# Performance work log

Hardware: AMD Instinct MI355X
Metric: run time of the kernel (lower is better)

The kernel has to match this reference:

```python
import jax, jax.numpy as jnp
import numpy as np
from jax import lax

B, T, A = 64, 1024, 512
FILTERS, K = 32, 31
PAD = (K - 1) // 2


def setup_inputs() -> dict:
    key = jax.random.key(0)
    ks = jax.random.split(key, 12)
    return {
        "encoder_seq_proj": jax.random.normal(ks[0], (B, T, A), jnp.float32),
        "query": jax.random.normal(ks[1], (B, A), jnp.float32),
        "cumulative": jax.random.uniform(ks[2], (B, T), jnp.float32),
        "attention": jax.random.uniform(ks[3], (B, T), jnp.float32),
        "alpha": jax.random.uniform(ks[4], (B, T), jnp.float32),
        "conv_w": jax.random.normal(ks[5], (FILTERS, 2, K), jnp.float32) * 0.1,
        "L_w": jax.random.normal(ks[6], (A, FILTERS), jnp.float32) * 0.1,
        "L_b": jax.random.normal(ks[7], (A,), jnp.float32) * 0.1,
        "W_w": jax.random.normal(ks[8], (A, A), jnp.float32) * 0.05,
        "W_b": jax.random.normal(ks[9], (A,), jnp.float32) * 0.05,
        "v_w": jax.random.normal(ks[10], (1, A), jnp.float32) * 0.05,
        "t": 1,
        "phone_len": jax.random.randint(ks[11], (B,), 1, T + 1).astype(jnp.int64),
    }


def reference(encoder_seq_proj, query, cumulative, attention, alpha,
              conv_w, L_w, L_b, W_w, W_b, v_w, t, phone_len):
    # attention mask from phone lengths (set at init, reused each step)
    mask = (jnp.arange(T)[None, :] < phone_len[:, None]).astype(encoder_seq_proj.dtype)
    # processed query: [B, 1, A]
    pq = (query @ W_w.T + W_b)[:, None, :]
    # location features: stack cumulative + previous attention -> [B, 2, T]
    loc = jnp.stack([cumulative, attention], axis=1)
    conv_out = lax.conv_general_dilated(
        loc, conv_w, window_strides=(1,), padding=[(PAD, PAD)],
        dimension_numbers=("NCH", "OIH", "NCH"))  # [B, F, T]
    ploc = jnp.einsum("bft,af->bta", conv_out, L_w) + L_b  # [B, T, A]
    # additive energies -> [B, T]
    u = jnp.einsum("bta,a->bt", jnp.tanh(pq + encoder_seq_proj + ploc), v_w[0])
    s = jax.nn.sigmoid(u)
    scores = s / jnp.sum(s, axis=1, keepdims=True)
    att = scores * mask
    # forward-attention recursion (enable_forward_bias=True path)
    shift_alpha = jnp.pad(alpha[:, :-1], ((0, 0), (1, 0)))
    dual_alpha = jnp.pad(alpha[:, :-2], ((0, 0), (2, 0)))
    new_alpha = (shift_alpha + dual_alpha + alpha + 1e-7) * att
    new_alpha = new_alpha / jnp.sum(new_alpha, axis=-1, keepdims=True)
    return new_alpha[:, None, :]  # [B, 1, T]
```

## Files before the change

kernel.cpp:

```cpp
#include <hip/hip_runtime.h>

#define NB 64
#define NT 1024
#define NA 512
#define NF 32
#define KW 31
#define PADW 15
#define TB 32

typedef __fp16 half2v __attribute__((ext_vector_type(2)));

__device__ __forceinline__ float fast_tanh(float x) {
    float e = __builtin_amdgcn_exp2f(x * 2.885390081777927f);
    return 1.0f - 2.0f * __builtin_amdgcn_rcpf(1.0f + e);
}
__device__ __forceinline__ float fast_sigmoid(float u) {
    return __builtin_amdgcn_rcpf(1.0f + __builtin_amdgcn_exp2f(-u * 1.4426950408889634f));
}
__device__ __forceinline__ unsigned pkrtz(float a, float b) {
    half2v h = __builtin_amdgcn_cvt_pkrtz(a, b);
    return __builtin_bit_cast(unsigned, h);
}
__device__ __forceinline__ float fdot2u(unsigned cv, unsigned lw, float acc) {
#if __has_builtin(__builtin_amdgcn_fdot2)
    return __builtin_amdgcn_fdot2(__builtin_bit_cast(half2v, cv),
                                  __builtin_bit_cast(half2v, lw), acc, false);
#else
    half2v a = __builtin_bit_cast(half2v, cv), b = __builtin_bit_cast(half2v, lw);
    return acc + (float)a.x * (float)b.x + (float)a.y * (float)b.y;
#endif
}

__global__ __launch_bounds__(256) void lsa_pq(
    const float* __restrict__ query, const float* __restrict__ Ww,
    const float* __restrict__ Wb, const float* __restrict__ convw,
    float* __restrict__ pq, float* __restrict__ cwT)
{
    if (blockIdx.x == 0) {
        for (int i = threadIdx.x; i < NF * 2 * KW; i += 256) {
            int f = i / (2 * KW);
            int r = i - f * 2 * KW;
            int c = r / KW;
            int k = r - c * KW;
            cwT[(c * KW + k) * NF + f] = convw[i];
        }
    }
    __shared__ float qs[NA];
    int tid = threadIdx.x;
    int b = blockIdx.x >> 1;
    int a0 = (blockIdx.x & 1) * 256;
    qs[tid]       = query[b * NA + tid];
    qs[tid + 256] = query[b * NA + tid + 256];
    __syncthreads();
    int a = a0 + tid;
    const float4* wr = (const float4*)(Ww + (long)a * NA);
    float acc  = Wb[a];
    float acc2 = 0.f;
#pragma unroll 8
    for (int k = 0; k < NA / 4; ++k) {
        float4 w = wr[k];
        float4 q4 = *(const float4*)(qs + 4 * k);
        acc  += w.x * q4.x + w.y * q4.y;
        acc2 += w.z * q4.z + w.w * q4.w;
    }
    pq[b * NA + a] = acc + acc2;
}

__global__ __launch_bounds__(256, 4) void lsa_main(
    const float* __restrict__ enc, const float* __restrict__ cum,
    const float* __restrict__ att, const float* __restrict__ cwT,
    const float* __restrict__ Lw, const float* __restrict__ Lb,
    const float* __restrict__ vw, const float* __restrict__ pq,
    float* __restrict__ sout)
{
    __shared__ float cum_s[TB + 30];
    __shared__ float att_s[TB + 30];
    __shared__ unsigned cvsh[TB][20];
    __shared__ float wred[4][33];

    int tid = threadIdx.x;
    int b  = blockIdx.x >> 5;
    int t0 = (blockIdx.x & 31) * TB;

    int a0 = 2 * tid;
    const float4* lp = (const float4*)(Lw + (long)a0 * NF);
    float4 lf[16];
#pragma unroll
    for (int i = 0; i < 16; ++i) lf[i] = lp[i];
    float c0 = pq[b * NA + a0]     + Lb[a0];
    float c1 = pq[b * NA + a0 + 1] + Lb[a0 + 1];
    float vx = vw[a0], vy = vw[a0 + 1];

    if (tid < TB + 30) {
        int t = t0 - PADW + tid;
        bool ok = (t >= 0) && (t < NT);
        cum_s[tid] = ok ? cum[b * NT + t] : 0.f;
        att_s[tid] = ok ? att[b * NT + t] : 0.f;
    }

    unsigned h0[16], h1[16];
#pragma unroll
    for (int i = 0; i < 8; ++i) {
        h0[2 * i]     = pkrtz(lf[i].x, lf[i].y);
        h0[2 * i + 1] = pkrtz(lf[i].z, lf[i].w);
        h1[2 * i]     = pkrtz(lf[8 + i].x, lf[8 + i].y);
        h1[2 * i + 1] = pkrtz(lf[8 + i].z, lf[8 + i].w);
    }
    __syncthreads();

    {
        int lane = tid & 63;
        int tt = lane & 31;
        int fbu = __builtin_amdgcn_readfirstlane(tid >> 6) * 8;
        const float* cw = cwT + fbu;
        float acc[8] = {0, 0, 0, 0, 0, 0, 0, 0};
        for (int k = 0; k < KW; ++k) {
            float x0 = cum_s[tt + k];
            float x1 = att_s[tt + k];
#pragma unroll
            for (int f8 = 0; f8 < 8; ++f8) {
                acc[f8] = fmaf(x0, cw[k * NF + f8],
                          fmaf(x1, cw[(KW + k) * NF + f8], acc[f8]));
            }
        }
        if (lane < 32) {
            uint4 pk;
            pk.x = pkrtz(acc[0], acc[1]);
            pk.y = pkrtz(acc[2], acc[3]);
            pk.z = pkrtz(acc[4], acc[5]);
            pk.w = pkrtz(acc[6], acc[7]);
            *(uint4*)&cvsh[tt][fbu >> 1] = pk;
        }
    }
    __syncthreads();

    float p32[TB];
    const float* erow = enc + ((long)b * NT + t0) * NA + a0;
#pragma unroll
    for (int tt = 0; tt < TB; ++tt) {
        float2 e = *(const float2*)(erow + (long)tt * NA);
        float x0[2] = {c0 + e.x, 0.f};
        float x1[2] = {c1 + e.y, 0.f};
#pragma unroll
        for (int q = 0; q < 4; ++q) {
            uint4 cv = *(const uint4*)&cvsh[tt][4 * q];
            int p = q & 1;
            x0[p] = fdot2u(cv.x, h0[4 * q + 0], x0[p]);
            x0[p] = fdot2u(cv.y, h0[4 * q + 1], x0[p]);
            x0[p] = fdot2u(cv.z, h0[4 * q + 2], x0[p]);
            x0[p] = fdot2u(cv.w, h0[4 * q + 3], x0[p]);
            x1[p] = fdot2u(cv.x, h1[4 * q + 0], x1[p]);
            x1[p] = fdot2u(cv.y, h1[4 * q + 1], x1[p]);
            x1[p] = fdot2u(cv.z, h1[4 * q + 2], x1[p]);
            x1[p] = fdot2u(cv.w, h1[4 * q + 3], x1[p]);
        }
        p32[tt] = fast_tanh(x0[0] + x0[1]) * vx + fast_tanh(x1[0] + x1[1]) * vy;
    }

    {
        int lane = tid & 63;
        int wv   = tid >> 6;
        int len = TB;
#pragma unroll
        for (int m = 1; m <= 16; m <<= 1) {
            int half = len >> 1;
            bool up = (lane & m) != 0;
#pragma unroll
            for (int i = 0; i < 16; ++i) {
                if (i < half) {
                    float send = up ? p32[i] : p32[i + half];
                    float keep = up ? p32[i + half] : p32[i];
                    p32[i] = keep + __shfl_xor(send, m, 64);
                }
            }
            len = half;
        }
        float v = p32[0] + __shfl_xor(p32[0], 32, 64);
        int l = lane & 31;
        int tt = ((l & 1) << 4) | ((l & 2) << 2) | (l & 4) | ((l & 8) >> 2) | ((l & 16) >> 4);
        if (lane < 32) wred[wv][tt] = v;
    }
    __syncthreads();
    if (tid < 32) {
        float u = wred[0][tid] + wred[1][tid] + wred[2][tid] + wred[3][tid];
        sout[b * NT + t0 + tid] = fast_sigmoid(u);
    }
}

__global__ __launch_bounds__(256) void lsa_norm(
    const float* __restrict__ alpha, const int* __restrict__ plen,
    float* __restrict__ out)
{
    __shared__ float red[4];
    int tid = threadIdx.x;
    int b = blockIdx.x;
    int pl = plen[b];
    float w[4];
    float psum = 0.f;
#pragma unroll
    for (int j = 0; j < 4; ++j) {
        int t = tid + 256 * j;
        float s   = out[b * NT + t];
        float al  = alpha[b * NT + t];
        float am1 = (t >= 1) ? alpha[b * NT + t - 1] : 0.f;
        float am2 = (t >= 2) ? alpha[b * NT + t - 2] : 0.f;
        float val = (t < pl) ? (al + am1 + am2 + 1e-7f) * s : 0.f;
        w[j] = val;
        psum += val;
    }
#pragma unroll
    for (int m = 32; m >= 1; m >>= 1) psum += __shfl_xor(psum, m, 64);
    int lane = tid & 63, wid = tid >> 6;
    if (lane == 0) red[wid] = psum;
    __syncthreads();
    float total = red[0] + red[1] + red[2] + red[3];
    float inv = 1.0f / total;
#pragma unroll
    for (int j = 0; j < 4; ++j) {
        int t = tid + 256 * j;
        out[b * NT + t] = w[j] * inv;
    }
}

extern "C" void kernel_launch(void* const* d_in, const int* in_sizes, int n_in,
                              void* d_out, int out_size, void* d_ws, size_t ws_size,
                              hipStream_t stream)
{
    const float* enc   = (const float*)d_in[0];
    const float* query = (const float*)d_in[1];
    const float* cum   = (const float*)d_in[2];
    const float* att   = (const float*)d_in[3];
    const float* alpha = (const float*)d_in[4];
    const float* convw = (const float*)d_in[5];
    const float* Lw    = (const float*)d_in[6];
    const float* Lb    = (const float*)d_in[7];
    const float* Ww    = (const float*)d_in[8];
    const float* Wb    = (const float*)d_in[9];
    const float* vw    = (const float*)d_in[10];
    const int*   plen  = (const int*)d_in[12];

    float* pq  = (float*)d_ws;
    float* cwT = (float*)d_ws + NB * NA;
    float* sout = (float*)d_out;

    lsa_pq  <<<NB * 2,         256, 0, stream>>>(query, Ww, Wb, convw, pq, cwT);
    lsa_main<<<NB * (NT / TB), 256, 0, stream>>>(enc, cum, att, cwT, Lw, Lb, vw, pq, sout);
    lsa_norm<<<NB,             256, 0, stream>>>(alpha, plen, sout);
}
```

Measured before the change: 70.23 us.

## Give each thread four attention columns over half the time rows, stage conv weights in LDS

Each wave of the main kernel now covers 256 attention columns and 16 of the 32 time rows. Each lane handles four consecutive columns with float4 encoder loads, so every conv-feature LDS read feeds four dot products instead of two. The conv weights are copied into shared memory and read as float4 with the tap loop fully unrolled, and the cross-lane reduction gets a shorter butterfly plus extra xor steps. The cost is twice as many packed weight registers, so the occupancy hint drops from 4 to 3 blocks per CU.

```diff
diff --git a/kernel.cpp b/kernel.cpp
--- a/kernel.cpp
+++ b/kernel.cpp
@@ -7,6 +7,7 @@
 #define KW 31
 #define PADW 15
 #define TB 32
+#define CWN (2 * KW * NF)
 
 typedef __fp16 half2v __attribute__((ext_vector_type(2)));
 
@@ -66,31 +67,37 @@
     pq[b * NA + a] = acc + acc2;
 }
 
-__global__ __launch_bounds__(256, 4) void lsa_main(
+__global__ __launch_bounds__(256, 3) void lsa_main(
     const float* __restrict__ enc, const float* __restrict__ cum,
     const float* __restrict__ att, const float* __restrict__ cwT,
     const float* __restrict__ Lw, const float* __restrict__ Lb,
     const float* __restrict__ vw, const float* __restrict__ pq,
     float* __restrict__ sout)
 {
+    __shared__ float cw_s[CWN];
     __shared__ float cum_s[TB + 30];
     __shared__ float att_s[TB + 30];
     __shared__ unsigned cvsh[TB][20];
-    __shared__ float wred[4][33];
-
-    int tid = threadIdx.x;
-    int b  = blockIdx.x >> 5;
-    int t0 = (blockIdx.x & 31) * TB;
-
-    int a0 = 2 * tid;
-    const float4* lp = (const float4*)(Lw + (long)a0 * NF);
-    float4 lf[16];
-#pragma unroll
-    for (int i = 0; i < 16; ++i) lf[i] = lp[i];
-    float c0 = pq[b * NA + a0]     + Lb[a0];
-    float c1 = pq[b * NA + a0 + 1] + Lb[a0 + 1];
-    float vx = vw[a0], vy = vw[a0 + 1];
-
+    __shared__ float wred[2][33];
+
+    int tid  = threadIdx.x;
+    int lane = tid & 63;
+    int wv   = tid >> 6;
+    int b    = blockIdx.x >> 5;
+    int t0   = (blockIdx.x & 31) * TB;
+
+    int ah = wv >> 1;
+    int th = wv & 1;
+    int a0 = ah * 256 + 4 * lane;
+
+    {
+        const float4* src = (const float4*)cwT;
+        float4* dst = (float4*)cw_s;
+        if (tid < 248) {
+            dst[tid]       = src[tid];
+            dst[tid + 248] = src[tid + 248];
+        }
+    }
     if (tid < TB + 30) {
         int t = t0 - PADW + tid;
         bool ok = (t >= 0) && (t < NT);
@@ -98,29 +105,46 @@
         att_s[tid] = ok ? att[b * NT + t] : 0.f;
     }
 
-    unsigned h0[16], h1[16];
-#pragma unroll
-    for (int i = 0; i < 8; ++i) {
-        h0[2 * i]     = pkrtz(lf[i].x, lf[i].y);
-        h0[2 * i + 1] = pkrtz(lf[i].z, lf[i].w);
-        h1[2 * i]     = pkrtz(lf[8 + i].x, lf[8 + i].y);
-        h1[2 * i + 1] = pkrtz(lf[8 + i].z, lf[8 + i].w);
-    }
-    __syncthreads();
-
-    {
-        int lane = tid & 63;
-        int tt = lane & 31;
-        int fbu = __builtin_amdgcn_readfirstlane(tid >> 6) * 8;
-        const float* cw = cwT + fbu;
+    unsigned h0[16], h1[16], h2[16], h3[16];
+    {
+        const float4* l0 = (const float4*)(Lw + (long)(a0 + 0) * NF);
+        const float4* l1 = (const float4*)(Lw + (long)(a0 + 1) * NF);
+        const float4* l2 = (const float4*)(Lw + (long)(a0 + 2) * NF);
+        const float4* l3 = (const float4*)(Lw + (long)(a0 + 3) * NF);
+#pragma unroll
+        for (int q = 0; q < 8; ++q) {
+            float4 w0 = l0[q], w1 = l1[q], w2 = l2[q], w3 = l3[q];
+            h0[2 * q] = pkrtz(w0.x, w0.y); h0[2 * q + 1] = pkrtz(w0.z, w0.w);
+            h1[2 * q] = pkrtz(w1.x, w1.y); h1[2 * q + 1] = pkrtz(w1.z, w1.w);
+            h2[2 * q] = pkrtz(w2.x, w2.y); h2[2 * q + 1] = pkrtz(w2.z, w2.w);
+            h3[2 * q] = pkrtz(w3.x, w3.y); h3[2 * q + 1] = pkrtz(w3.z, w3.w);
+        }
+    }
+    float4 c4 = *(const float4*)(pq + b * NA + a0);
+    {
+        float4 lb4 = *(const float4*)(Lb + a0);
+        c4.x += lb4.x; c4.y += lb4.y; c4.z += lb4.z; c4.w += lb4.w;
+    }
+    float4 v4 = *(const float4*)(vw + a0);
+    __syncthreads();
+
+    {
+        int tt  = lane & 31;
+        int fbu = wv * 8;
         float acc[8] = {0, 0, 0, 0, 0, 0, 0, 0};
+#pragma unroll
         for (int k = 0; k < KW; ++k) {
             float x0 = cum_s[tt + k];
             float x1 = att_s[tt + k];
-#pragma unroll
-            for (int f8 = 0; f8 < 8; ++f8) {
-                acc[f8] = fmaf(x0, cw[k * NF + f8],
-                          fmaf(x1, cw[(KW + k) * NF + f8], acc[f8]));
+            const float4* A  = (const float4*)(cw_s + k * NF + fbu);
+            const float4* Bv = (const float4*)(cw_s + (KW + k) * NF + fbu);
+#pragma unroll
+            for (int j = 0; j < 2; ++j) {
+                float4 wa = A[j], wb = Bv[j];
+                acc[4 * j + 0] = fmaf(x0, wa.x, fmaf(x1, wb.x, acc[4 * j + 0]));
+                acc[4 * j + 1] = fmaf(x0, wa.y, fmaf(x1, wb.y, acc[4 * j + 1]));
+                acc[4 * j + 2] = fmaf(x0, wa.z, fmaf(x1, wb.z, acc[4 * j + 2]));
+                acc[4 * j + 3] = fmaf(x0, wa.w, fmaf(x1, wb.w, acc[4 * j + 3]));
             }
         }
         if (lane < 32) {
@@ -134,55 +158,64 @@
     }
     __syncthreads();
 
-    float p32[TB];
-    const float* erow = enc + ((long)b * NT + t0) * NA + a0;
-#pragma unroll
-    for (int tt = 0; tt < TB; ++tt) {
-        float2 e = *(const float2*)(erow + (long)tt * NA);
-        float x0[2] = {c0 + e.x, 0.f};
-        float x1[2] = {c1 + e.y, 0.f};
-#pragma unroll
-        for (int q = 0; q < 4; ++q) {
-            uint4 cv = *(const uint4*)&cvsh[tt][4 * q];
-            int p = q & 1;
-            x0[p] = fdot2u(cv.x, h0[4 * q + 0], x0[p]);
-            x0[p] = fdot2u(cv.y, h0[4 * q + 1], x0[p]);
-            x0[p] = fdot2u(cv.z, h0[4 * q + 2], x0[p]);
-            x0[p] = fdot2u(cv.w, h0[4 * q + 3], x0[p]);
-            x1[p] = fdot2u(cv.x, h1[4 * q + 0], x1[p]);
-            x1[p] = fdot2u(cv.y, h1[4 * q + 1], x1[p]);
-            x1[p] = fdot2u(cv.z, h1[4 * q + 2], x1[p]);
-            x1[p] = fdot2u(cv.w, h1[4 * q + 3], x1[p]);
-        }
-        p32[tt] = fast_tanh(x0[0] + x0[1]) * vx + fast_tanh(x1[0] + x1[1]) * vy;
-    }
-
-    {
-        int lane = tid & 63;
-        int wv   = tid >> 6;
-        int len = TB;
-#pragma unroll
-        for (int m = 1; m <= 16; m <<= 1) {
+#define DOROW(hr, cinit, vmul)                                      \
+    {                                                               \
+        float ya = (cinit), yb = 0.f;                               \
+        ya = fdot2u(cva.x, hr[0],  ya); yb = fdot2u(cva.y, hr[1],  yb); \
+        ya = fdot2u(cva.z, hr[2],  ya); yb = fdot2u(cva.w, hr[3],  yb); \
+        ya = fdot2u(cvb.x, hr[4],  ya); yb = fdot2u(cvb.y, hr[5],  yb); \
+        ya = fdot2u(cvb.z, hr[6],  ya); yb = fdot2u(cvb.w, hr[7],  yb); \
+        ya = fdot2u(cvc.x, hr[8],  ya); yb = fdot2u(cvc.y, hr[9],  yb); \
+        ya = fdot2u(cvc.z, hr[10], ya); yb = fdot2u(cvc.w, hr[11], yb); \
+        ya = fdot2u(cvd.x, hr[12], ya); yb = fdot2u(cvd.y, hr[13], yb); \
+        ya = fdot2u(cvd.z, hr[14], ya); yb = fdot2u(cvd.w, hr[15], yb); \
+        s = fmaf(fast_tanh(ya + yb), (vmul), s);                    \
+    }
+
+    float p[16];
+    const float* erow = enc + ((long)b * NT + t0 + th * 16) * NA + a0;
+#pragma unroll
+    for (int tt = 0; tt < 16; ++tt) {
+        int gtt = th * 16 + tt;
+        float4 e = *(const float4*)(erow + (long)tt * NA);
+        uint4 cva = *(const uint4*)&cvsh[gtt][0];
+        uint4 cvb = *(const uint4*)&cvsh[gtt][4];
+        uint4 cvc = *(const uint4*)&cvsh[gtt][8];
+        uint4 cvd = *(const uint4*)&cvsh[gtt][12];
+        float s = 0.f;
+        DOROW(h0, c4.x + e.x, v4.x);
+        DOROW(h1, c4.y + e.y, v4.y);
+        DOROW(h2, c4.z + e.z, v4.z);
+        DOROW(h3, c4.w + e.w, v4.w);
+        p[tt] = s;
+    }
+#undef DOROW
+
+    {
+        int len = 16;
+#pragma unroll
+        for (int m = 1; m <= 8; m <<= 1) {
             int half = len >> 1;
             bool up = (lane & m) != 0;
 #pragma unroll
-            for (int i = 0; i < 16; ++i) {
+            for (int i = 0; i < 8; ++i) {
                 if (i < half) {
-                    float send = up ? p32[i] : p32[i + half];
-                    float keep = up ? p32[i + half] : p32[i];
-                    p32[i] = keep + __shfl_xor(send, m, 64);
+                    float send = up ? p[i] : p[i + half];
+                    float keep = up ? p[i + half] : p[i];
+                    p[i] = keep + __shfl_xor(send, m, 64);
                 }
             }
             len = half;
         }
-        float v = p32[0] + __shfl_xor(p32[0], 32, 64);
-        int l = lane & 31;
-        int tt = ((l & 1) << 4) | ((l & 2) << 2) | (l & 4) | ((l & 8) >> 2) | ((l & 16) >> 4);
-        if (lane < 32) wred[wv][tt] = v;
+        float v = p[0] + __shfl_xor(p[0], 16, 64);
+        v = v + __shfl_xor(v, 32, 64);
+        int l4 = lane & 15;
+        int tt = ((l4 & 1) << 3) | ((l4 & 2) << 1) | ((l4 & 4) >> 1) | ((l4 & 8) >> 3);
+        if (lane < 16) wred[ah][th * 16 + tt] = v;
     }
     __syncthreads();
     if (tid < 32) {
-        float u = wred[0][tid] + wred[1][tid] + wred[2][tid] + wred[3][tid];
+        float u = wred[0][tid] + wred[1][tid];
         sout[b * NT + t0 + tid] = fast_sigmoid(u);
     }
 }
```

After: 118.9 us. +69.4%, slower.

## Process 64 timesteps per block and stage conv weights in shared memory

Applied to the files above, without the earlier changes.

Each block of the main kernel now covers 64 timesteps instead of 32, halving the block count. Per-block setup (loading the L weight rows into registers, converting them to fp16, loading pq/bias) is now amortised over twice as many timesteps. The conv weights are staged into LDS and read as float4, and all 64 lanes of each wave now do useful conv work instead of only half. The trade-off is more LDS per block, two sequential 32-step passes, and fewer blocks to spread across the GPU.

```diff
diff --git a/kernel.cpp b/kernel.cpp
--- a/kernel.cpp
+++ b/kernel.cpp
@@ -6,7 +6,8 @@
 #define NF 32
 #define KW 31
 #define PADW 15
-#define TB 32
+#define TC 64
+#define CWN (2 * KW * NF)
 
 typedef __fp16 half2v __attribute__((ext_vector_type(2)));
 
@@ -73,14 +74,32 @@
     const float* __restrict__ vw, const float* __restrict__ pq,
     float* __restrict__ sout)
 {
-    __shared__ float cum_s[TB + 30];
-    __shared__ float att_s[TB + 30];
-    __shared__ unsigned cvsh[TB][20];
-    __shared__ float wred[4][33];
-
-    int tid = threadIdx.x;
-    int b  = blockIdx.x >> 5;
-    int t0 = (blockIdx.x & 31) * TB;
+    __shared__ float cw_s[CWN];
+    __shared__ float cum_s[TC + 30];
+    __shared__ float att_s[TC + 30];
+    __shared__ unsigned cvsh[TC][20];
+    __shared__ float wred[4][TC + 2];
+
+    int tid  = threadIdx.x;
+    int lane = tid & 63;
+    int wv   = tid >> 6;
+    int b    = blockIdx.x >> 4;
+    int t0   = (blockIdx.x & 15) * TC;
+
+    {
+        const float4* src = (const float4*)cwT;
+        float4* dst = (float4*)cw_s;
+        if (tid < 248) {
+            dst[tid]       = src[tid];
+            dst[tid + 248] = src[tid + 248];
+        }
+    }
+    if (tid < TC + 30) {
+        int t = t0 - PADW + tid;
+        bool ok = (t >= 0) && (t < NT);
+        cum_s[tid] = ok ? cum[b * NT + t] : 0.f;
+        att_s[tid] = ok ? att[b * NT + t] : 0.f;
+    }
 
     int a0 = 2 * tid;
     const float4* lp = (const float4*)(Lw + (long)a0 * NF);
@@ -90,13 +109,6 @@
     float c0 = pq[b * NA + a0]     + Lb[a0];
     float c1 = pq[b * NA + a0 + 1] + Lb[a0 + 1];
     float vx = vw[a0], vy = vw[a0 + 1];
-
-    if (tid < TB + 30) {
-        int t = t0 - PADW + tid;
-        bool ok = (t >= 0) && (t < NT);
-        cum_s[tid] = ok ? cum[b * NT + t] : 0.f;
-        att_s[tid] = ok ? att[b * NT + t] : 0.f;
-    }
 
     unsigned h0[16], h1[16];
 #pragma unroll
@@ -109,79 +121,83 @@
     __syncthreads();
 
     {
-        int lane = tid & 63;
-        int tt = lane & 31;
-        int fbu = __builtin_amdgcn_readfirstlane(tid >> 6) * 8;
-        const float* cw = cwT + fbu;
+        int tt  = lane;
+        int fbu = wv * 8;
         float acc[8] = {0, 0, 0, 0, 0, 0, 0, 0};
+#pragma unroll
         for (int k = 0; k < KW; ++k) {
             float x0 = cum_s[tt + k];
             float x1 = att_s[tt + k];
-#pragma unroll
-            for (int f8 = 0; f8 < 8; ++f8) {
-                acc[f8] = fmaf(x0, cw[k * NF + f8],
-                          fmaf(x1, cw[(KW + k) * NF + f8], acc[f8]));
+            const float4* A  = (const float4*)(cw_s + k * NF + fbu);
+            const float4* Bv = (const float4*)(cw_s + (KW + k) * NF + fbu);
+#pragma unroll
+            for (int j = 0; j < 2; ++j) {
+                float4 wa = A[j], wb = Bv[j];
+                acc[4 * j + 0] = fmaf(x0, wa.x, fmaf(x1, wb.x, acc[4 * j + 0]));
+                acc[4 * j + 1] = fmaf(x0, wa.y, fmaf(x1, wb.y, acc[4 * j + 1]));
+                acc[4 * j + 2] = fmaf(x0, wa.z, fmaf(x1, wb.z, acc[4 * j + 2]));
+                acc[4 * j + 3] = fmaf(x0, wa.w, fmaf(x1, wb.w, acc[4 * j + 3]));
             }
         }
-        if (lane < 32) {
-            uint4 pk;
-            pk.x = pkrtz(acc[0], acc[1]);
-            pk.y = pkrtz(acc[2], acc[3]);
-            pk.z = pkrtz(acc[4], acc[5]);
-            pk.w = pkrtz(acc[6], acc[7]);
-            *(uint4*)&cvsh[tt][fbu >> 1] = pk;
-        }
-    }
-    __syncthreads();
-
-    float p32[TB];
+        uint4 pk;
+        pk.x = pkrtz(acc[0], acc[1]);
+        pk.y = pkrtz(acc[2], acc[3]);
+        pk.z = pkrtz(acc[4], acc[5]);
+        pk.w = pkrtz(acc[6], acc[7]);
+        *(uint4*)&cvsh[tt][wv * 4] = pk;
+    }
+    __syncthreads();
+
     const float* erow = enc + ((long)b * NT + t0) * NA + a0;
-#pragma unroll
-    for (int tt = 0; tt < TB; ++tt) {
-        float2 e = *(const float2*)(erow + (long)tt * NA);
-        float x0[2] = {c0 + e.x, 0.f};
-        float x1[2] = {c1 + e.y, 0.f};
-#pragma unroll
-        for (int q = 0; q < 4; ++q) {
-            uint4 cv = *(const uint4*)&cvsh[tt][4 * q];
-            int p = q & 1;
-            x0[p] = fdot2u(cv.x, h0[4 * q + 0], x0[p]);
-            x0[p] = fdot2u(cv.y, h0[4 * q + 1], x0[p]);
-            x0[p] = fdot2u(cv.z, h0[4 * q + 2], x0[p]);
-            x0[p] = fdot2u(cv.w, h0[4 * q + 3], x0[p]);
-            x1[p] = fdot2u(cv.x, h1[4 * q + 0], x1[p]);
-            x1[p] = fdot2u(cv.y, h1[4 * q + 1], x1[p]);
-            x1[p] = fdot2u(cv.z, h1[4 * q + 2], x1[p]);
-            x1[p] = fdot2u(cv.w, h1[4 * q + 3], x1[p]);
-        }
-        p32[tt] = fast_tanh(x0[0] + x0[1]) * vx + fast_tanh(x1[0] + x1[1]) * vy;
-    }
-
-    {
-        int lane = tid & 63;
-        int wv   = tid >> 6;
-        int len = TB;
-#pragma unroll
-        for (int m = 1; m <= 16; m <<= 1) {
-            int half = len >> 1;
-            bool up = (lane & m) != 0;
-#pragma unroll
-            for (int i = 0; i < 16; ++i) {
-                if (i < half) {
-                    float send = up ? p32[i] : p32[i + half];
-                    float keep = up ? p32[i + half] : p32[i];
-                    p32[i] = keep + __shfl_xor(send, m, 64);
+#pragma unroll 1
+    for (int half = 0; half < 2; ++half) {
+        float p32[32];
+#pragma unroll
+        for (int tt = 0; tt < 32; ++tt) {
+            int gtt = half * 32 + tt;
+            float2 e = *(const float2*)(erow + (long)gtt * NA);
+            float x0[2] = {c0 + e.x, 0.f};
+            float x1[2] = {c1 + e.y, 0.f};
+#pragma unroll
+            for (int q = 0; q < 4; ++q) {
+                uint4 cv = *(const uint4*)&cvsh[gtt][4 * q];
+                int p = q & 1;
+                x0[p] = fdot2u(cv.x, h0[4 * q + 0], x0[p]);
+                x0[p] = fdot2u(cv.y, h0[4 * q + 1], x0[p]);
+                x0[p] = fdot2u(cv.z, h0[4 * q + 2], x0[p]);
+                x0[p] = fdot2u(cv.w, h0[4 * q + 3], x0[p]);
+                x1[p] = fdot2u(cv.x, h1[4 * q + 0], x1[p]);
+                x1[p] = fdot2u(cv.y, h1[4 * q + 1], x1[p]);
+                x1[p] = fdot2u(cv.z, h1[4 * q + 2], x1[p]);
+                x1[p] = fdot2u(cv.w, h1[4 * q + 3], x1[p]);
+            }
+            p32[tt] = fast_tanh(x0[0] + x0[1]) * vx + fast_tanh(x1[0] + x1[1]) * vy;
+        }
+
+        {
+            int len = 32;
+#pragma unroll
+            for (int m = 1; m <= 16; m <<= 1) {
+                int hlen = len >> 1;
+                bool up = (lane & m) != 0;
+#pragma unroll
+                for (int i = 0; i < 16; ++i) {
+                    if (i < hlen) {
+                        float send = up ? p32[i] : p32[i + hlen];
+                        float keep = up ? p32[i + hlen] : p32[i];
+                        p32[i] = keep + __shfl_xor(send, m, 64);
+                    }
                 }
+                len = hlen;
             }
-            len = half;
-        }
-        float v = p32[0] + __shfl_xor(p32[0], 32, 64);
-        int l = lane & 31;
-        int tt = ((l & 1) << 4) | ((l & 2) << 2) | (l & 4) | ((l & 8) >> 2) | ((l & 16) >> 4);
-        if (lane < 32) wred[wv][tt] = v;
-    }
-    __syncthreads();
-    if (tid < 32) {
+            float v = p32[0] + __shfl_xor(p32[0], 32, 64);
+            int l = lane & 31;
+            int tt = ((l & 1) << 4) | ((l & 2) << 2) | (l & 4) | ((l & 8) >> 2) | ((l & 16) >> 4);
+            if (lane < 32) wred[wv][half * 32 + tt] = v;
+        }
+    }
+    __syncthreads();
+    if (tid < TC) {
         float u = wred[0][tid] + wred[1][tid] + wred[2][tid] + wred[3][tid];
         sout[b * NT + t0 + tid] = fast_sigmoid(u);
     }
@@ -244,6 +260,6 @@
     float* sout = (float*)d_out;
 
     lsa_pq  <<<NB * 2,         256, 0, stream>>>(query, Ww, Wb, convw, pq, cwT);
-    lsa_main<<<NB * (NT / TB), 256, 0, stream>>>(enc, cum, att, cwT, Lw, Lb, vw, pq, sout);
+    lsa_main<<<NB * (NT / TC), 256, 0, stream>>>(enc, cum, att, cwT, Lw, Lb, vw, pq, sout);
     lsa_norm<<<NB,             256, 0, stream>>>(alpha, plen, sout);
 }
```

Result: faster. 63.72 us (-9.3%).
